# Performance work log

Hardware: AMD Instinct MI355X
Metric: run time of the kernel (lower is better)

## Reference

```python
import jax, jax.numpy as jnp
import numpy as np

N_NODES = 50000
N_EDGES = 800000
D_IN = 96
D_OUT = 96


def setup_inputs() -> dict:
    key = jax.random.key(0)
    k1, k2, k3 = jax.random.split(key, 3)
    x = jax.random.normal(k1, (N_NODES, D_IN), dtype=jnp.float32)
    edge_index = jax.random.randint(k2, (2, N_EDGES), 0, N_NODES, dtype=jnp.int64)
    edge_weight = jnp.ones((N_EDGES,), dtype=jnp.float32)
    # Glorot-ish init for the linear weight, zero bias (as in PyG GCNConv)
    W = jax.random.normal(k3, (D_IN, D_OUT), dtype=jnp.float32) * (1.0 / np.sqrt(D_IN))
    b = jnp.zeros((D_OUT,), dtype=jnp.float32)
    return {"x": x, "edge_index": edge_index, "edge_weight": edge_weight, "W": W, "b": b}


def reference(x, edge_index, edge_weight, W, b):
    """PyG GCNConv: out = D^{-1/2} (A + I) D^{-1/2} (x @ W) + b."""
    N = x.shape[0]
    row, col = edge_index[0], edge_index[1]  # source -> target
    # add self loops with weight 1 (PyG default add_self_loops=True)
    loop = jnp.arange(N, dtype=edge_index.dtype)
    row = jnp.concatenate([row, loop])
    col = jnp.concatenate([col, loop])
    ew = jnp.concatenate([edge_weight, jnp.ones((N,), dtype=edge_weight.dtype)])
    # symmetric normalization based on (weighted) in-degree over col
    deg = jax.ops.segment_sum(ew, col, num_segments=N)  # [N]
    dinv = jnp.where(deg > 0, jax.lax.rsqrt(deg), 0.0)
    norm = dinv[row] * ew * dinv[col]  # [E+N]
    # linear transform first (small GEMM), then gather-scale-scatter over edges
    h = x @ W  # [N, D_OUT]
    msg = h[row] * norm[:, None]  # [E+N, D_OUT]
    out = jax.ops.segment_sum(msg, col, num_segments=N)  # [N, D_OUT]
    return out + b
```

## Files before the change

### kernel.cpp

```cpp
#include <hip/hip_runtime.h>

#define N_NODES 50000
#define N_EDGES 800000
#define D 96
#define NBKT 256
#define BNODES 196
#define BCAP 4608
#define PART_B 250
#define EPB (N_EDGES / PART_B)
#define CAP 48
#define GCAP 1536

typedef float vfloat4 __attribute__((ext_vector_type(4)));

__device__ __forceinline__ float bf_lo(unsigned u) { return __uint_as_float(u << 16); }
__device__ __forceinline__ float bf_hi(unsigned u) { return __uint_as_float(u & 0xFFFF0000u); }
__device__ __forceinline__ unsigned f2bf_bits(unsigned u) {
    return (u + 0x7FFFu + ((u >> 16) & 1u)) & 0xFFFF0000u;
}

__device__ __forceinline__ int exscan256(int v, int* wsum) {
    int lane = threadIdx.x & 63;
    int wave = threadIdx.x >> 6;
    int incl = v;
#pragma unroll
    for (int off = 1; off < 64; off <<= 1) {
        int t = __shfl_up(incl, off);
        if (lane >= off) incl += t;
    }
    if (lane == 63) wsum[wave] = incl;
    __syncthreads();
    int base = 0;
#pragma unroll
    for (int wv = 0; wv < 3; ++wv) base += (wv < wave) ? wsum[wv] : 0;
    return base + incl - v;
}

__global__ __launch_bounds__(256) void k_part(const int* __restrict__ row,
                                              const int* __restrict__ col,
                                              const float* __restrict__ ew,
                                              int* __restrict__ bkt_cnt,
                                              uint2* __restrict__ bktbuf) {
    __shared__ int hist[NBKT];
    __shared__ int cur[NBKT];
    int tid = threadIdx.x;
    hist[tid] = 0;
    __syncthreads();
    int e0 = blockIdx.x * EPB;
    for (int i = tid; i < EPB; i += 256)
        atomicAdd(&hist[col[e0 + i] / BNODES], 1);
    __syncthreads();
    cur[tid] = atomicAdd(&bkt_cnt[tid], hist[tid]);
    __syncthreads();
    for (int i = tid; i < EPB; i += 256) {
        int e = e0 + i;
        int c = col[e];
        int b = c / BNODES;
        int p = atomicAdd(&cur[b], 1);
        if (p < BCAP)
            bktbuf[(size_t)b * BCAP + p] =
                make_uint2((unsigned)row[e] | ((unsigned)(c - b * BNODES) << 16),
                           __float_as_uint(ew[e]));
    }
}

__global__ __launch_bounds__(256) void k_bin(const int* __restrict__ bkt_cnt,
                                             const uint2* __restrict__ bktbuf,
                                             unsigned* __restrict__ recs,
                                             int* __restrict__ rowptr,
                                             float* __restrict__ dinv) {
    __shared__ int wsum1[4];
    __shared__ int wsum2[4];
    __shared__ int sbkt[NBKT];
    __shared__ int lcnt[BNODES];
    __shared__ int loff[256];
    __shared__ unsigned lslot[BNODES * CAP];
    int tid = threadIdx.x;
    int b = blockIdx.x;

    int bv = min(bkt_cnt[tid], BCAP);
    int bex = exscan256(bv, wsum1);
    sbkt[tid] = bex;
    for (int i = tid; i < BNODES; i += 256) lcnt[i] = 0;
    __syncthreads();
    int gbase = sbkt[b];
    int ne = min(bkt_cnt[b], BCAP);

    for (int i = tid; i < ne; i += 256) {
        uint2 r = bktbuf[(size_t)b * BCAP + i];
        int lc = (int)(r.x >> 16);
        int p = atomicAdd(&lcnt[lc], 1);
        if (p < CAP) lslot[lc * CAP + p] = f2bf_bits(r.y) | (r.x & 0xFFFFu);
    }
    __syncthreads();

    int myv = (tid < BNODES) ? min(lcnt[tid], CAP) : 0;
    int ex2 = exscan256(myv, wsum2);
    loff[tid] = ex2;
    __syncthreads();

    for (int i = tid; i < BNODES * CAP; i += 256) {
        int ln = i / CAP, s = i % CAP;
        if (s < min(lcnt[ln], CAP))
            recs[gbase + loff[ln] + s] = lslot[i];
    }
    int base = b * BNODES;
    for (int i = tid; i < BNODES; i += 256) {
        int n = base + i;
        if (n <= N_NODES) rowptr[n] = gbase + loff[i];
        if (n < N_NODES) {
            int cn = min(lcnt[i], CAP);
            float d = 1.0f;
            for (int k = 0; k < cn; ++k) d += bf_hi(lslot[i * CAP + k]);
            dinv[n] = rsqrtf(d);
        }
    }
}

__global__ __launch_bounds__(256) void k_gemm(const float* __restrict__ x,
                                              const float* __restrict__ W,
                                              const float* __restrict__ dinv,
                                              unsigned short* __restrict__ hb) {
    __shared__ float Wl[D * D];
    int tid = threadIdx.x;
    const float4* Wg4 = (const float4*)W;
    float4* Wl4 = (float4*)Wl;
    for (int i = tid; i < D * D / 4; i += 256) Wl4[i] = Wg4[i];
    __syncthreads();

    int jg = tid % 24;
    int ng = tid / 24;
    bool active = (ng < 10);
    int j = jg * 4;
    int node0 = blockIdx.x * 40 + ng * 4;

    float acc[4][4] = {};
    if (active) {
        for (int k4 = 0; k4 < D / 4; ++k4) {
            float4 xv[4];
#pragma unroll
            for (int i = 0; i < 4; ++i)
                xv[i] = *(const float4*)&x[(node0 + i) * D + k4 * 4];
#pragma unroll
            for (int kk = 0; kk < 4; ++kk) {
                float4 w4 = *(const float4*)&Wl[(k4 * 4 + kk) * D + j];
#pragma unroll
                for (int i = 0; i < 4; ++i) {
                    float xs = (kk == 0) ? xv[i].x : (kk == 1) ? xv[i].y
                             : (kk == 2) ? xv[i].z : xv[i].w;
                    acc[i][0] += xs * w4.x;
                    acc[i][1] += xs * w4.y;
                    acc[i][2] += xs * w4.z;
                    acc[i][3] += xs * w4.w;
                }
            }
        }
#pragma unroll
        for (int i = 0; i < 4; ++i) {
            int n = node0 + i;
            float di = dinv[n];
            ushort4 pk;
            pk.x = (unsigned short)(f2bf_bits(__float_as_uint(acc[i][0] * di)) >> 16);
            pk.y = (unsigned short)(f2bf_bits(__float_as_uint(acc[i][1] * di)) >> 16);
            pk.z = (unsigned short)(f2bf_bits(__float_as_uint(acc[i][2] * di)) >> 16);
            pk.w = (unsigned short)(f2bf_bits(__float_as_uint(acc[i][3] * di)) >> 16);
            *(ushort4*)&hb[(size_t)n * D + j] = pk;
        }
    }
}

__global__ __launch_bounds__(192) void k_gather(const int* __restrict__ rowptr,
                                                const unsigned* __restrict__ recs,
                                                const unsigned short* __restrict__ hb,
                                                const float* __restrict__ dinv,
                                                const float* __restrict__ bias,
                                                float* __restrict__ out) {
    __shared__ unsigned sre[GCAP];
    __shared__ int sptr[17];
    int tid = threadIdx.x;
    int nb = blockIdx.x * 16;

    if (tid < 17) sptr[tid] = rowptr[nb + tid];
    __syncthreads();
    int e0 = sptr[0];
    int stage = min(sptr[16] - e0, GCAP);
    for (int i = tid; i < stage; i += 192) sre[i] = recs[e0 + i];
    __syncthreads();

    int local = tid / 12;
    int jq = tid % 12;
    int n = nb + local;
    int j = jq * 8;

    uint4 sv = *(const uint4*)(hb + (size_t)n * D + j);
    float acc[8];
    acc[0] = bf_lo(sv.x); acc[1] = bf_hi(sv.x);
    acc[2] = bf_lo(sv.y); acc[3] = bf_hi(sv.y);
    acc[4] = bf_lo(sv.z); acc[5] = bf_hi(sv.z);
    acc[6] = bf_lo(sv.w); acc[7] = bf_hi(sv.w);

    int ls = sptr[local] - e0;
    int le = sptr[local + 1] - e0;
    int idx = ls;
    for (; idx + 2 <= le; idx += 2) {
        unsigned r0 = (idx < GCAP) ? sre[idx] : recs[e0 + idx];
        unsigned r1 = (idx + 1 < GCAP) ? sre[idx + 1] : recs[e0 + idx + 1];
        uint4 v0 = *(const uint4*)(hb + (size_t)(r0 & 0xFFFFu) * D + j);
        uint4 v1 = *(const uint4*)(hb + (size_t)(r1 & 0xFFFFu) * D + j);
        float w0 = bf_hi(r0), w1 = bf_hi(r1);
        acc[0] += w0 * bf_lo(v0.x); acc[1] += w0 * bf_hi(v0.x);
        acc[2] += w0 * bf_lo(v0.y); acc[3] += w0 * bf_hi(v0.y);
        acc[4] += w0 * bf_lo(v0.z); acc[5] += w0 * bf_hi(v0.z);
        acc[6] += w0 * bf_lo(v0.w); acc[7] += w0 * bf_hi(v0.w);
        acc[0] += w1 * bf_lo(v1.x); acc[1] += w1 * bf_hi(v1.x);
        acc[2] += w1 * bf_lo(v1.y); acc[3] += w1 * bf_hi(v1.y);
        acc[4] += w1 * bf_lo(v1.z); acc[5] += w1 * bf_hi(v1.z);
        acc[6] += w1 * bf_lo(v1.w); acc[7] += w1 * bf_hi(v1.w);
    }
    if (idx < le) {
        unsigned r0 = (idx < GCAP) ? sre[idx] : recs[e0 + idx];
        uint4 v0 = *(const uint4*)(hb + (size_t)(r0 & 0xFFFFu) * D + j);
        float w0 = bf_hi(r0);
        acc[0] += w0 * bf_lo(v0.x); acc[1] += w0 * bf_hi(v0.x);
        acc[2] += w0 * bf_lo(v0.y); acc[3] += w0 * bf_hi(v0.y);
        acc[4] += w0 * bf_lo(v0.z); acc[5] += w0 * bf_hi(v0.z);
        acc[6] += w0 * bf_lo(v0.w); acc[7] += w0 * bf_hi(v0.w);
    }

    float di = dinv[n];
    float4 b0 = *(const float4*)&bias[j];
    float4 b1 = *(const float4*)&bias[j + 4];
    vfloat4 o0, o1;
    o0.x = acc[0] * di + b0.x; o0.y = acc[1] * di + b0.y;
    o0.z = acc[2] * di + b0.z; o0.w = acc[3] * di + b0.w;
    o1.x = acc[4] * di + b1.x; o1.y = acc[5] * di + b1.y;
    o1.z = acc[6] * di + b1.z; o1.w = acc[7] * di + b1.w;
    __builtin_nontemporal_store(o0, (vfloat4*)&out[(size_t)n * D + j]);
    __builtin_nontemporal_store(o1, (vfloat4*)&out[(size_t)n * D + j + 4]);
}

extern "C" void kernel_launch(void* const* d_in, const int* in_sizes, int n_in,
                              void* d_out, int out_size, void* d_ws, size_t ws_size,
                              hipStream_t stream) {
    const float* x  = (const float*)d_in[0];
    const int*   ei = (const int*)d_in[1];
    const float* ew = (const float*)d_in[2];
    const float* W  = (const float*)d_in[3];
    const float* b  = (const float*)d_in[4];
    float* out = (float*)d_out;

    const int* row = ei;
    const int* col = ei + N_EDGES;

    char* p = (char*)d_ws;
    unsigned short* hb     = (unsigned short*)p;
    uint2*          bktbuf = (uint2*)p;            p += (size_t)N_NODES * D * 2;
    unsigned*       recs   = (unsigned*)p;         p += (size_t)N_EDGES * 4;
    int*            rowptr = (int*)p;              p += (size_t)(N_NODES + 16) * 4;
    float*          dinv   = (float*)p;            p += (size_t)N_NODES * 4;
    int*            bkt_cnt= (int*)p;              p += (size_t)NBKT * 4;

    (void)hipMemsetAsync(bkt_cnt, 0, NBKT * sizeof(int), stream);
    k_part  <<<PART_B, 256, 0, stream>>>(row, col, ew, bkt_cnt, bktbuf);
    k_bin   <<<NBKT, 256, 0, stream>>>(bkt_cnt, bktbuf, recs, rowptr, dinv);
    k_gemm  <<<1250, 256, 0, stream>>>(x, W, dinv, hb);
    k_gather<<<(N_NODES + 15) / 16, 192, 0, stream>>>(rowptr, recs, hb, dinv, b, out);
}
```

Measured before the change: 152.8 us.

## Compact bin records in LDS, prefetch partition columns, unroll gather by four

k_part now loads each thread's column indices into registers once and reuses them for both the histogram and scatter passes. k_bin compacts the per-node slot array in shared memory through a register round-trip, then writes the records out contiguously instead of through a strided masked loop. The gather kernel drops the global-memory fallback, halves its LDS staging buffer (relying on CAP bounding 16 nodes to 768 records) and unrolls the edge loop by four for more loads in flight. The GEMM switches x to nontemporal loads. The cost is higher register pressure from the unrolled arrays, which may reduce occupancy.

```diff
diff --git a/kernel.cpp b/kernel.cpp
--- a/kernel.cpp
+++ b/kernel.cpp
@@ -8,8 +8,11 @@
 #define BCAP 4608
 #define PART_B 250
 #define EPB (N_EDGES / PART_B)
+#define EPT 13
 #define CAP 48
-#define GCAP 1536
+#define NSLOT (BNODES * CAP)
+#define KDUMP 37
+#define GCAP 768
 
 typedef float vfloat4 __attribute__((ext_vector_type(4)));
 
@@ -47,20 +50,32 @@
     hist[tid] = 0;
     __syncthreads();
     int e0 = blockIdx.x * EPB;
-    for (int i = tid; i < EPB; i += 256)
-        atomicAdd(&hist[col[e0 + i] / BNODES], 1);
+
+    int myc[EPT];
+#pragma unroll
+    for (int k = 0; k < EPT; ++k) {
+        int i = tid + 256 * k;
+        myc[k] = (i < EPB) ? col[e0 + i] : -1;
+    }
+#pragma unroll
+    for (int k = 0; k < EPT; ++k)
+        if (myc[k] >= 0) atomicAdd(&hist[myc[k] / BNODES], 1);
     __syncthreads();
     cur[tid] = atomicAdd(&bkt_cnt[tid], hist[tid]);
     __syncthreads();
-    for (int i = tid; i < EPB; i += 256) {
-        int e = e0 + i;
-        int c = col[e];
-        int b = c / BNODES;
-        int p = atomicAdd(&cur[b], 1);
-        if (p < BCAP)
-            bktbuf[(size_t)b * BCAP + p] =
-                make_uint2((unsigned)row[e] | ((unsigned)(c - b * BNODES) << 16),
-                           __float_as_uint(ew[e]));
+#pragma unroll
+    for (int k = 0; k < EPT; ++k) {
+        int i = tid + 256 * k;
+        if (myc[k] >= 0) {
+            int e = e0 + i;
+            int c = myc[k];
+            int b = c / BNODES;
+            int p = atomicAdd(&cur[b], 1);
+            if (p < BCAP)
+                bktbuf[(size_t)b * BCAP + p] =
+                    make_uint2((unsigned)row[e] | ((unsigned)(c - b * BNODES) << 16),
+                               __float_as_uint(ew[e]));
+        }
     }
 }
 
@@ -74,7 +89,8 @@
     __shared__ int sbkt[NBKT];
     __shared__ int lcnt[BNODES];
     __shared__ int loff[256];
-    __shared__ unsigned lslot[BNODES * CAP];
+    __shared__ int stot;
+    __shared__ unsigned lslot[NSLOT];
     int tid = threadIdx.x;
     int b = blockIdx.x;
 
@@ -97,21 +113,39 @@
     int myv = (tid < BNODES) ? min(lcnt[tid], CAP) : 0;
     int ex2 = exscan256(myv, wsum2);
     loff[tid] = ex2;
-    __syncthreads();
-
-    for (int i = tid; i < BNODES * CAP; i += 256) {
-        int ln = i / CAP, s = i % CAP;
-        if (s < min(lcnt[ln], CAP))
-            recs[gbase + loff[ln] + s] = lslot[i];
-    }
+    if (tid == 255) stot = ex2;
+    __syncthreads();
+
+    unsigned vals[KDUMP];
+    int dst[KDUMP];
+#pragma unroll
+    for (int k = 0; k < KDUMP; ++k) {
+        int i = tid + 256 * k;
+        bool in = i < NSLOT;
+        int ln = in ? i / CAP : 0;
+        int s = in ? i % CAP : 0;
+        bool act = in && (s < min(lcnt[ln], CAP));
+        vals[k] = act ? lslot[i] : 0u;
+        dst[k] = act ? (loff[ln] + s) : -1;
+    }
+    __syncthreads();
+#pragma unroll
+    for (int k = 0; k < KDUMP; ++k)
+        if (dst[k] >= 0) lslot[dst[k]] = vals[k];
+    __syncthreads();
+
+    int tot = stot;
+    for (int i = tid; i < tot; i += 256) recs[gbase + i] = lslot[i];
+
     int base = b * BNODES;
     for (int i = tid; i < BNODES; i += 256) {
         int n = base + i;
         if (n <= N_NODES) rowptr[n] = gbase + loff[i];
         if (n < N_NODES) {
             int cn = min(lcnt[i], CAP);
+            int o = loff[i];
             float d = 1.0f;
-            for (int k = 0; k < cn; ++k) d += bf_hi(lslot[i * CAP + k]);
+            for (int k = 0; k < cn; ++k) d += bf_hi(lslot[o + k]);
             dinv[n] = rsqrtf(d);
         }
     }
@@ -137,10 +171,11 @@
     float acc[4][4] = {};
     if (active) {
         for (int k4 = 0; k4 < D / 4; ++k4) {
-            float4 xv[4];
+            vfloat4 xv[4];
 #pragma unroll
             for (int i = 0; i < 4; ++i)
-                xv[i] = *(const float4*)&x[(node0 + i) * D + k4 * 4];
+                xv[i] = __builtin_nontemporal_load(
+                    (const vfloat4*)&x[(node0 + i) * D + k4 * 4]);
 #pragma unroll
             for (int kk = 0; kk < 4; ++kk) {
                 float4 w4 = *(const float4*)&Wl[(k4 * 4 + kk) * D + j];
@@ -183,7 +218,7 @@
     if (tid < 17) sptr[tid] = rowptr[nb + tid];
     __syncthreads();
     int e0 = sptr[0];
-    int stage = min(sptr[16] - e0, GCAP);
+    int stage = sptr[16] - e0;
     for (int i = tid; i < stage; i += 192) sre[i] = recs[e0 + i];
     __syncthreads();
 
@@ -202,12 +237,13 @@
     int ls = sptr[local] - e0;
     int le = sptr[local + 1] - e0;
     int idx = ls;
-    for (; idx + 2 <= le; idx += 2) {
-        unsigned r0 = (idx < GCAP) ? sre[idx] : recs[e0 + idx];
-        unsigned r1 = (idx + 1 < GCAP) ? sre[idx + 1] : recs[e0 + idx + 1];
+    for (; idx + 4 <= le; idx += 4) {
+        unsigned r0 = sre[idx], r1 = sre[idx + 1], r2 = sre[idx + 2], r3 = sre[idx + 3];
         uint4 v0 = *(const uint4*)(hb + (size_t)(r0 & 0xFFFFu) * D + j);
         uint4 v1 = *(const uint4*)(hb + (size_t)(r1 & 0xFFFFu) * D + j);
-        float w0 = bf_hi(r0), w1 = bf_hi(r1);
+        uint4 v2 = *(const uint4*)(hb + (size_t)(r2 & 0xFFFFu) * D + j);
+        uint4 v3 = *(const uint4*)(hb + (size_t)(r3 & 0xFFFFu) * D + j);
+        float w0 = bf_hi(r0), w1 = bf_hi(r1), w2 = bf_hi(r2), w3 = bf_hi(r3);
         acc[0] += w0 * bf_lo(v0.x); acc[1] += w0 * bf_hi(v0.x);
         acc[2] += w0 * bf_lo(v0.y); acc[3] += w0 * bf_hi(v0.y);
         acc[4] += w0 * bf_lo(v0.z); acc[5] += w0 * bf_hi(v0.z);
@@ -216,9 +252,17 @@
         acc[2] += w1 * bf_lo(v1.y); acc[3] += w1 * bf_hi(v1.y);
         acc[4] += w1 * bf_lo(v1.z); acc[5] += w1 * bf_hi(v1.z);
         acc[6] += w1 * bf_lo(v1.w); acc[7] += w1 * bf_hi(v1.w);
-    }
-    if (idx < le) {
-        unsigned r0 = (idx < GCAP) ? sre[idx] : recs[e0 + idx];
+        acc[0] += w2 * bf_lo(v2.x); acc[1] += w2 * bf_hi(v2.x);
+        acc[2] += w2 * bf_lo(v2.y); acc[3] += w2 * bf_hi(v2.y);
+        acc[4] += w2 * bf_lo(v2.z); acc[5] += w2 * bf_hi(v2.z);
+        acc[6] += w2 * bf_lo(v2.w); acc[7] += w2 * bf_hi(v2.w);
+        acc[0] += w3 * bf_lo(v3.x); acc[1] += w3 * bf_hi(v3.x);
+        acc[2] += w3 * bf_lo(v3.y); acc[3] += w3 * bf_hi(v3.y);
+        acc[4] += w3 * bf_lo(v3.z); acc[5] += w3 * bf_hi(v3.z);
+        acc[6] += w3 * bf_lo(v3.w); acc[7] += w3 * bf_hi(v3.w);
+    }
+    for (; idx < le; ++idx) {
+        unsigned r0 = sre[idx];
         uint4 v0 = *(const uint4*)(hb + (size_t)(r0 & 0xFFFFu) * D + j);
         float w0 = bf_hi(r0);
         acc[0] += w0 * bf_lo(v0.x); acc[1] += w0 * bf_hi(v0.x);
```

New measurement: 157.4 us. 3.0% more time.
